# Optimization experiments

Hardware: AMD Instinct MI355X
Metric: run time of the kernel (lower is better)

The kernel has to match this reference:

```python
import jax, jax.numpy as jnp
import numpy as np
import math

B, N, W = 8, 2048, 512

def setup_inputs() -> dict:
    key0 = jax.random.key(0)
    ks = jax.random.split(key0, 6)
    return {
        "query": jax.random.normal(ks[0], (B, N, W), dtype=jnp.float32),
        "key":   jax.random.normal(ks[1], (B, N, W), dtype=jnp.float32),
        "W1": jax.random.normal(ks[2], (W, W), dtype=jnp.float32) * (1.0 / math.sqrt(W)),
        "b1": jax.random.normal(ks[3], (W,), dtype=jnp.float32) * 0.01,
        "W2": jax.random.normal(ks[4], (W, W), dtype=jnp.float32) * (1.0 / math.sqrt(W)),
        "b2": jax.random.normal(ks[5], (W,), dtype=jnp.float32) * 0.01,
    }

def _attn(q, k, v):
    # scores: [B, N, N]
    d_k = q.shape[-1]
    scores = jnp.einsum('bnd,bmd->bnm', q, k) / jnp.sqrt(jnp.asarray(d_k, q.dtype))
    p = jax.nn.softmax(scores, axis=-1)
    return jnp.einsum('bnm,bmd->bnd', p, v)

def reference(query, key, W1, b1, W2, b2):
    # nn.Linear: x @ W.T + b
    q = jnp.einsum('bnd,ed->bne', query, W1) + b1
    k = jnp.einsum('bnd,ed->bne', key, W2) + b2
    x1 = _attn(q, k, q)  # attention(query, key, query)
    x2 = _attn(k, q, k)  # attention(key, query, key)
    return jnp.concatenate((x1, x2), axis=1)  # [B, 2N, W]
```

## Files before the change

kernel.cpp:

```cpp
#include <hip/hip_runtime.h>
#include <hip/hip_bf16.h>
#include <stdint.h>

typedef unsigned short ushort_t;
typedef __attribute__((ext_vector_type(8))) short short8;
typedef __attribute__((ext_vector_type(4))) short short4v;
typedef __attribute__((ext_vector_type(4))) float f32x4;

__device__ inline ushort_t f2bf(float x) {
  uint32_t u = __float_as_uint(x);
  u += 0x7fffu + ((u >> 16) & 1u);
  return (ushort_t)(u >> 16);
}
__device__ inline float bfu2f(uint32_t h) { return __uint_as_float(h << 16); }

__device__ inline uint32_t pk2bf(float a, float b) {
  __hip_bfloat162 h = __float22bfloat162_rn(make_float2(a, b));
  union { __hip_bfloat162 h2; uint32_t u; } cv; cv.h2 = h; return cv.u;
}

__device__ inline void gload_lds16(const void* g, void* l) {
  __builtin_amdgcn_global_load_lds((const __attribute__((address_space(1))) uint32_t*)g,
                                   (__attribute__((address_space(3))) uint32_t*)l, 16, 0, 0);
}

__global__ __launch_bounds__(256) void linear_kernel(
    const float* __restrict__ query, const float* __restrict__ key,
    const float* __restrict__ W1, const float* __restrict__ b1,
    const float* __restrict__ W2, const float* __restrict__ b2,
    ushort_t* __restrict__ q_bf, ushort_t* __restrict__ k_bf,
    ushort_t* __restrict__ qT, ushort_t* __restrict__ kT)
{
  extern __shared__ __attribute__((aligned(16))) char smraw[];
  float*    smF = (float*)smraw;
  ushort_t* smU = (ushort_t*)smraw;

  int bx0 = blockIdx.x;
  int bx = ((bx0 & 7) << 7) | (bx0 >> 3);

  int which = bx >> 9, r2 = bx & 511, ct = r2 & 3, rt = r2 >> 2;
  const float* X    = which ? key : query;
  const float* Wm   = which ? W2  : W1;
  const float* bias = which ? b2  : b1;
  ushort_t* OUT  = which ? k_bf : q_bf;
  ushort_t* OUTT = which ? kT   : qT;

  int t = threadIdx.x, w = t >> 6, lane = t & 63, g = lane >> 4, m = lane & 15;
  int wr = (w >> 1) * 64, wc = (w & 1) * 64;
  int sr = lane >> 3, sp = lane & 7, sc = sp ^ sr;

  f32x4 zero = {0.f, 0.f, 0.f, 0.f};
  f32x4 acc[4][4];
#pragma unroll
  for (int i = 0; i < 4; ++i)
#pragma unroll
    for (int j = 0; j < 4; ++j) acc[i][j] = zero;

  auto stage = [&](int buf, int d0) {
    float* dst = smF + buf * 8192;
#pragma unroll
    for (int i = 0; i < 8; ++i) {
      int qi = w * 8 + i;
      const float* gsrc;
      float* ldst;
      if (qi < 16) {
        gsrc = X + (size_t)(rt * 128 + qi * 8 + sr) * 512 + d0 + sc * 4;
        ldst = dst + qi * 256;
      } else {
        int s = qi - 16;
        gsrc = Wm + (size_t)(ct * 128 + s * 8 + sr) * 512 + d0 + sc * 4;
        ldst = dst + 4096 + s * 256;
      }
      gload_lds16(gsrc, ldst);
    }
  };

  stage(0, 0);

  for (int it = 0; it < 16; ++it) {
    int cur = it & 1;
    __syncthreads();
    if (it + 1 < 16) stage(1 - cur, (it + 1) * 32);
    const float* bufF = smF + cur * 8192;

    short8 a4[4], b4[4];
#pragma unroll
    for (int i = 0; i < 4; ++i) {
      int row = wr + 16 * i + m, r8 = row & 7;
      int base = (row >> 3) * 256 + r8 * 32;
      f32x4 lo = *(const f32x4*)&bufF[base + (((2 * g)     ^ r8) * 4)];
      f32x4 hi = *(const f32x4*)&bufF[base + (((2 * g + 1) ^ r8) * 4)];
      union { uint32_t u[4]; short8 s; } fr;
      fr.u[0] = pk2bf(lo[0], lo[1]); fr.u[1] = pk2bf(lo[2], lo[3]);
      fr.u[2] = pk2bf(hi[0], hi[1]); fr.u[3] = pk2bf(hi[2], hi[3]);
      a4[i] = fr.s;
    }
#pragma unroll
    for (int j = 0; j < 4; ++j) {
      int row = wc + 16 * j + m, r8 = row & 7;
      int base = 4096 + (row >> 3) * 256 + r8 * 32;
      f32x4 lo = *(const f32x4*)&bufF[base + (((2 * g)     ^ r8) * 4)];
      f32x4 hi = *(const f32x4*)&bufF[base + (((2 * g + 1) ^ r8) * 4)];
      union { uint32_t u[4]; short8 s; } fr;
      fr.u[0] = pk2bf(lo[0], lo[1]); fr.u[1] = pk2bf(lo[2], lo[3]);
      fr.u[2] = pk2bf(hi[0], hi[1]); fr.u[3] = pk2bf(hi[2], hi[3]);
      b4[j] = fr.s;
    }
#pragma unroll
    for (int i = 0; i < 4; ++i)
#pragma unroll
      for (int j = 0; j < 4; ++j)
        acc[i][j] = __builtin_amdgcn_mfma_f32_16x16x32_bf16(a4[i], b4[j], acc[i][j], 0, 0, 0);
  }
  __syncthreads();

  float bw[4];
#pragma unroll
  for (int j = 0; j < 4; ++j) bw[j] = bias[ct * 128 + wc + 16 * j + m];

#pragma unroll
  for (int j = 0; j < 4; ++j)
#pragma unroll
    for (int i = 0; i < 4; ++i) {
      f32x4 c4 = acc[i][j];
#pragma unroll
      for (int rr = 0; rr < 4; ++rr)
        smU[(wr + 16 * i + 4 * g + rr) * 136 + wc + 16 * j + m] = f2bf(c4[rr] + bw[j]);
    }
  __syncthreads();
  {
    int row = t >> 1, half = t & 1;
    size_t gb = (size_t)(rt * 128 + row) * 512 + ct * 128 + half * 64;
#pragma unroll
    for (int i = 0; i < 8; ++i)
      *(short8*)(OUT + gb + i * 8) = *(const short8*)&smU[row * 136 + half * 64 + i * 8];
  }
  __syncthreads();

#pragma unroll
  for (int j = 0; j < 4; ++j)
#pragma unroll
    for (int i = 0; i < 4; ++i) {
      f32x4 c4 = acc[i][j];
      short4v tv;
#pragma unroll
      for (int rr = 0; rr < 4; ++rr) tv[rr] = (short)f2bf(c4[rr] + bw[j]);
      *(short4v*)&smU[(wc + 16 * j + m) * 136 + wr + 16 * i + 4 * g] = tv;
    }
  __syncthreads();
  {
    int cC = t >> 1, half = t & 1;
    size_t b_ = (size_t)(rt >> 4);
    size_t gb = b_ * (512 * 2048) + (size_t)(ct * 128 + cC) * 2048
              + (size_t)(rt & 15) * 128 + half * 64;
#pragma unroll
    for (int i = 0; i < 8; ++i)
      *(short8*)(OUTT + gb + i * 8) = *(const short8*)&smU[cC * 136 + half * 64 + i * 8];
  }
}

__global__ __launch_bounds__(512, 2) void attn_kernel(
    const ushort_t* __restrict__ qb, const ushort_t* __restrict__ kb_,
    const ushort_t* __restrict__ qT, const ushort_t* __restrict__ kT,
    float* __restrict__ out)
{
  extern __shared__ ushort_t sm[];
  const float CEXP = 1.4426950408889634f / 22.62741699796952f;

  int bx = blockIdx.x;
  int group = bx & 15, mtile = bx >> 4;
  int b = group >> 1, att = group & 1;
  const ushort_t* Qp = (att ? kb_ : qb) + (size_t)b * (2048 * 512);
  const ushort_t* Kp = (att ? qb  : kb_) + (size_t)b * (2048 * 512);
  const ushort_t* Vt = (att ? kT  : qT)  + (size_t)b * (512 * 2048);

  int t = threadIdx.x, w = t >> 6, lane = t & 63, g = lane >> 4, m = lane & 15;
  int wq = w >> 1, dh = w & 1;
  int qrow = mtile * 128 + w * 16 + m;
  int sw8  = ((g ^ ((m >> 1) & 3)) * 8);
  int srow = lane >> 2;
  int soff = ((lane & 3) ^ ((lane >> 3) & 3)) * 8;
  int pm6 = (m & 6);

  ushort_t* Plds = sm + 65536;
  float* lbuf = (float*)(sm + 69632);

  int pw0 = (w * 16 + m) * 32 + ((g ^ pm6) << 2);
  int pw1 = (w * 16 + m) * 32 + (((g + 4) ^ pm6) << 2);
  int pr0 = (wq * 32 +      m) * 32 + (((2 * g) ^ pm6) << 2);
  int pr1 = (wq * 32 + 16 + m) * 32 + (((2 * g) ^ pm6) << 2);

  short8 qf[16];
#pragma unroll
  for (int ks = 0; ks < 16; ++ks)
    qf[ks] = *(const short8*)(Qp + (size_t)qrow * 512 + ks * 32 + g * 8);

  f32x4 zero = {0.f, 0.f, 0.f, 0.f};
  f32x4 acc[16][2];
#pragma unroll
  for (int dt = 0; dt < 16; ++dt) { acc[dt][0] = zero; acc[dt][1] = zero; }
  float l = 0.f;

  auto stage = [&](int buf, int kb) {
    ushort_t* base = sm + buf * 32768;
    const int kbase = kb * 32;
#pragma unroll
    for (int i = 0; i < 4; ++i) {
      int qi = w * 4 + i, ks = qi >> 1, tt2 = qi & 1;
      const ushort_t* gsrc = Kp + (size_t)(kbase + tt2 * 16 + srow) * 512 + ks * 32 + soff;
      gload_lds16(gsrc, base + ks * 1024 + tt2 * 512);
    }
#pragma unroll
    for (int i = 0; i < 4; ++i) {
      int qi = w * 4 + i;
      const ushort_t* gsrc = Vt + (size_t)(qi * 16 + srow) * 2048 + kbase + soff;
      gload_lds16(gsrc, base + 16384 + qi * 512);
    }
  };

  stage(0, 0);

  for (int kb = 0; kb < 64; ++kb) {
    int cur = kb & 1;
    __syncthreads();
    if (kb + 1 < 64) stage(1 - cur, kb + 1);
    const ushort_t* base = sm + cur * 32768;

    f32x4 T0 = zero, T1 = zero;
    __builtin_amdgcn_s_setprio(1);
#pragma unroll
    for (int ks = 0; ks < 16; ++ks) {
      short8 k0 = *(const short8*)&base[ks * 1024 +       m * 32 + sw8];
      short8 k1 = *(const short8*)&base[ks * 1024 + 512 + m * 32 + sw8];
      T0 = __builtin_amdgcn_mfma_f32_16x16x32_bf16(k0, qf[ks], T0, 0, 0, 0);
      T1 = __builtin_amdgcn_mfma_f32_16x16x32_bf16(k1, qf[ks], T1, 0, 0, 0);
    }
    __builtin_amdgcn_s_setprio(0);

    uint32_t h[8];
#pragma unroll
    for (int r = 0; r < 4; ++r) {
      float e0 = __builtin_amdgcn_exp2f(T0[r] * CEXP);
      float e1 = __builtin_amdgcn_exp2f(T1[r] * CEXP);
      h[r]     = f2bf(e0);
      h[4 + r] = f2bf(e1);
      l += bfu2f(h[r]) + bfu2f(h[4 + r]);
    }
    uint2 p0, p1;
    p0.x = h[0] | (h[1] << 16); p0.y = h[2] | (h[3] << 16);
    p1.x = h[4] | (h[5] << 16); p1.y = h[6] | (h[7] << 16);
    *(uint2*)&Plds[pw0] = p0;
    *(uint2*)&Plds[pw1] = p1;

    __syncthreads();

    short8 pf0 = *(const short8*)&Plds[pr0];
    short8 pf1 = *(const short8*)&Plds[pr1];
    __builtin_amdgcn_s_setprio(1);
#pragma unroll
    for (int dt = 0; dt < 16; ++dt) {
      short8 vf = *(const short8*)&base[16384 + (dh * 16 + dt) * 512 + m * 32 + sw8];
      acc[dt][0] = __builtin_amdgcn_mfma_f32_16x16x32_bf16(vf, pf0, acc[dt][0], 0, 0, 0);
      acc[dt][1] = __builtin_amdgcn_mfma_f32_16x16x32_bf16(vf, pf1, acc[dt][1], 0, 0, 0);
    }
    __builtin_amdgcn_s_setprio(0);
  }

  l += __shfl_xor(l, 16, 64);
  l += __shfl_xor(l, 32, 64);
  if (lane < 16) lbuf[w * 16 + lane] = 1.0f / l;
  __syncthreads();

  float inv0 = lbuf[wq * 32 + m];
  float inv1 = lbuf[wq * 32 + 16 + m];
  size_t orow0 = (size_t)b * 4096 + (size_t)att * 2048 + mtile * 128 + wq * 32 + m;
  float* ob0 = out + orow0 * 512 + dh * 256;
  float* ob1 = out + (orow0 + 16) * 512 + dh * 256;
#pragma unroll
  for (int dt = 0; dt < 16; ++dt) {
    f32x4 v0 = acc[dt][0] * inv0;
    *(f32x4*)(ob0 + dt * 16 + g * 4) = v0;
  }
#pragma unroll
  for (int dt = 0; dt < 16; ++dt) {
    f32x4 v1 = acc[dt][1] * inv1;
    *(f32x4*)(ob1 + dt * 16 + g * 4) = v1;
  }
}

extern "C" void kernel_launch(void* const* d_in, const int* in_sizes, int n_in,
                              void* d_out, int out_size, void* d_ws, size_t ws_size,
                              hipStream_t stream) {
  const float* query = (const float*)d_in[0];
  const float* key   = (const float*)d_in[1];
  const float* W1    = (const float*)d_in[2];
  const float* b1    = (const float*)d_in[3];
  const float* W2    = (const float*)d_in[4];
  const float* b2    = (const float*)d_in[5];
  float* out = (float*)d_out;

  ushort_t* ws   = (ushort_t*)d_ws;
  ushort_t* q_bf = ws;
  ushort_t* k_bf = ws + 8388608;
  ushort_t* qT   = ws + 16777216;
  ushort_t* kT   = ws + 25165824;

  (void)hipFuncSetAttribute((const void*)linear_kernel,
                            hipFuncAttributeMaxDynamicSharedMemorySize, 65536);
  (void)hipFuncSetAttribute((const void*)attn_kernel,
                            hipFuncAttributeMaxDynamicSharedMemorySize, 139776);

  linear_kernel<<<1024, 256, 65536, stream>>>(query, key, W1, b1, W2, b2,
                                              q_bf, k_bf, qT, kT);
  attn_kernel<<<256, 512, 139776, stream>>>(q_bf, k_bf, qT, kT, out);
}
```

Before: 311.0 us.

## Software-pipeline PV of previous tile behind QK and retile PV per wave

Splits K and V staging into separate double buffers and double-buffers the P tile in LDS. Each iteration computes QK for the current key tile, then runs the P·V product of the previous tile, which removes the mid-iteration barrier between writing P and consuming it. The P·V work per wave changes from 16 d-tiles by 2 q-tiles to 8 d-tiles by 4 q-tiles, so each V fragment loaded from LDS feeds more MFMAs. The cost is more LDS, more accumulator and P-fragment registers, and an extra drain step after the loop.

```diff
diff --git a/kernel.cpp b/kernel.cpp
--- a/kernel.cpp
+++ b/kernel.cpp
@@ -175,20 +175,23 @@
   const ushort_t* Vt = (att ? kT  : qT)  + (size_t)b * (512 * 2048);
 
   int t = threadIdx.x, w = t >> 6, lane = t & 63, g = lane >> 4, m = lane & 15;
-  int wq = w >> 1, dh = w & 1;
+  int dq = w >> 1, qh = w & 1;
   int qrow = mtile * 128 + w * 16 + m;
   int sw8  = ((g ^ ((m >> 1) & 3)) * 8);
   int srow = lane >> 2;
   int soff = ((lane & 3) ^ ((lane >> 3) & 3)) * 8;
   int pm6 = (m & 6);
 
-  ushort_t* Plds = sm + 65536;
-  float* lbuf = (float*)(sm + 69632);
+  ushort_t* Plds = sm + 131072 / 2 * 2;
+  float* lbuf = (float*)(sm + 73728);
+  (void)Plds;
 
   int pw0 = (w * 16 + m) * 32 + ((g ^ pm6) << 2);
   int pw1 = (w * 16 + m) * 32 + (((g + 4) ^ pm6) << 2);
-  int pr0 = (wq * 32 +      m) * 32 + (((2 * g) ^ pm6) << 2);
-  int pr1 = (wq * 32 + 16 + m) * 32 + (((2 * g) ^ pm6) << 2);
+  int prq[4];
+#pragma unroll
+  for (int qt = 0; qt < 4; ++qt)
+    prq[qt] = (qh * 64 + qt * 16 + m) * 32 + (((2 * g) ^ pm6) << 2);
 
   short8 qf[16];
 #pragma unroll
@@ -196,46 +199,73 @@
     qf[ks] = *(const short8*)(Qp + (size_t)qrow * 512 + ks * 32 + g * 8);
 
   f32x4 zero = {0.f, 0.f, 0.f, 0.f};
-  f32x4 acc[16][2];
-#pragma unroll
-  for (int dt = 0; dt < 16; ++dt) { acc[dt][0] = zero; acc[dt][1] = zero; }
+  f32x4 acc[8][4];
+#pragma unroll
+  for (int dt = 0; dt < 8; ++dt)
+#pragma unroll
+    for (int qt = 0; qt < 4; ++qt) acc[dt][qt] = zero;
   float l = 0.f;
 
-  auto stage = [&](int buf, int kb) {
-    ushort_t* base = sm + buf * 32768;
-    const int kbase = kb * 32;
+  auto stageK = [&](int buf, int kt) {
+    ushort_t* base = sm + buf * 16384;
+    const int kbase = kt * 32;
 #pragma unroll
     for (int i = 0; i < 4; ++i) {
       int qi = w * 4 + i, ks = qi >> 1, tt2 = qi & 1;
       const ushort_t* gsrc = Kp + (size_t)(kbase + tt2 * 16 + srow) * 512 + ks * 32 + soff;
       gload_lds16(gsrc, base + ks * 1024 + tt2 * 512);
     }
+  };
+  auto stageV = [&](int buf, int kt) {
+    ushort_t* base = sm + 32768 + buf * 16384;
+    const int kbase = kt * 32;
 #pragma unroll
     for (int i = 0; i < 4; ++i) {
       int qi = w * 4 + i;
       const ushort_t* gsrc = Vt + (size_t)(qi * 16 + srow) * 2048 + kbase + soff;
-      gload_lds16(gsrc, base + 16384 + qi * 512);
+      gload_lds16(gsrc, base + qi * 512);
     }
   };
 
-  stage(0, 0);
+  auto pv = [&](int pt) {
+    int pb = pt & 1;
+    const ushort_t* vb = sm + 32768 + pb * 16384;
+    const ushort_t* pp = sm + 65536 + pb * 4096;
+    short8 pf[4];
+#pragma unroll
+    for (int qt = 0; qt < 4; ++qt) pf[qt] = *(const short8*)&pp[prq[qt]];
+    __builtin_amdgcn_s_setprio(1);
+#pragma unroll
+    for (int dt = 0; dt < 8; ++dt) {
+      short8 vf = *(const short8*)&vb[(dq * 8 + dt) * 512 + m * 32 + sw8];
+#pragma unroll
+      for (int qt = 0; qt < 4; ++qt)
+        acc[dt][qt] = __builtin_amdgcn_mfma_f32_16x16x32_bf16(vf, pf[qt], acc[dt][qt], 0, 0, 0);
+    }
+    __builtin_amdgcn_s_setprio(0);
+  };
+
+  stageK(0, 0);
 
   for (int kb = 0; kb < 64; ++kb) {
     int cur = kb & 1;
     __syncthreads();
-    if (kb + 1 < 64) stage(1 - cur, kb + 1);
-    const ushort_t* base = sm + cur * 32768;
-
+    if (kb + 1 < 64) stageK(1 - cur, kb + 1);
+    stageV(cur, kb);
+
+    const ushort_t* kbuf = sm + cur * 16384;
     f32x4 T0 = zero, T1 = zero;
     __builtin_amdgcn_s_setprio(1);
 #pragma unroll
     for (int ks = 0; ks < 16; ++ks) {
-      short8 k0 = *(const short8*)&base[ks * 1024 +       m * 32 + sw8];
-      short8 k1 = *(const short8*)&base[ks * 1024 + 512 + m * 32 + sw8];
+      short8 k0 = *(const short8*)&kbuf[ks * 1024 +       m * 32 + sw8];
+      short8 k1 = *(const short8*)&kbuf[ks * 1024 + 512 + m * 32 + sw8];
       T0 = __builtin_amdgcn_mfma_f32_16x16x32_bf16(k0, qf[ks], T0, 0, 0, 0);
       T1 = __builtin_amdgcn_mfma_f32_16x16x32_bf16(k1, qf[ks], T1, 0, 0, 0);
     }
     __builtin_amdgcn_s_setprio(0);
+
+    if (kb > 0) pv(kb - 1);
 
     uint32_t h[8];
 #pragma unroll
@@ -249,42 +279,30 @@
     uint2 p0, p1;
     p0.x = h[0] | (h[1] << 16); p0.y = h[2] | (h[3] << 16);
     p1.x = h[4] | (h[5] << 16); p1.y = h[6] | (h[7] << 16);
-    *(uint2*)&Plds[pw0] = p0;
-    *(uint2*)&Plds[pw1] = p1;
-
-    __syncthreads();
-
-    short8 pf0 = *(const short8*)&Plds[pr0];
-    short8 pf1 = *(const short8*)&Plds[pr1];
-    __builtin_amdgcn_s_setprio(1);
-#pragma unroll
-    for (int dt = 0; dt < 16; ++dt) {
-      short8 vf = *(const short8*)&base[16384 + (dh * 16 + dt) * 512 + m * 32 + sw8];
-      acc[dt][0] = __builtin_amdgcn_mfma_f32_16x16x32_bf16(vf, pf0, acc[dt][0], 0, 0, 0);
-      acc[dt][1] = __builtin_amdgcn_mfma_f32_16x16x32_bf16(vf, pf1, acc[dt][1], 0, 0, 0);
-    }
-    __builtin_amdgcn_s_setprio(0);
+    ushort_t* pwb = sm + 65536 + cur * 4096;
+    *(uint2*)&pwb[pw0] = p0;
+    *(uint2*)&pwb[pw1] = p1;
   }
 
   l += __shfl_xor(l, 16, 64);
   l += __shfl_xor(l, 32, 64);
   if (lane < 16) lbuf[w * 16 + lane] = 1.0f / l;
-  __syncthreads();
-
-  float inv0 = lbuf[wq * 32 + m];
-  float inv1 = lbuf[wq * 32 + 16 + m];
-  size_t orow0 = (size_t)b * 4096 + (size_t)att * 2048 + mtile * 128 + wq * 32 + m;
-  float* ob0 = out + orow0 * 512 + dh * 256;
-  float* ob1 = out + (orow0 + 16) * 512 + dh * 256;
-#pragma unroll
-  for (int dt = 0; dt < 16; ++dt) {
-    f32x4 v0 = acc[dt][0] * inv0;
-    *(f32x4*)(ob0 + dt * 16 + g * 4) = v0;
-  }
-#pragma unroll
-  for (int dt = 0; dt < 16; ++dt) {
-    f32x4 v1 = acc[dt][1] * inv1;
-    *(f32x4*)(ob1 + dt * 16 + g * 4) = v1;
+
+  __syncthreads();
+  pv(63);
+
+  float inv[4];
+#pragma unroll
+  for (int qt = 0; qt < 4; ++qt) inv[qt] = lbuf[qh * 64 + qt * 16 + m];
+  size_t orow = (size_t)b * 4096 + (size_t)att * 2048 + mtile * 128 + qh * 64 + m;
+#pragma unroll
+  for (int qt = 0; qt < 4; ++qt) {
+    float* ob = out + (orow + qt * 16) * 512 + dq * 128;
+#pragma unroll
+    for (int dt = 0; dt < 8; ++dt) {
+      f32x4 v = acc[dt][qt] * inv[qt];
+      *(f32x4*)(ob + dt * 16 + g * 4) = v;
+    }
   }
 }
 
@@ -308,9 +326,9 @@
   (void)hipFuncSetAttribute((const void*)linear_kernel,
                             hipFuncAttributeMaxDynamicSharedMemorySize, 65536);
   (void)hipFuncSetAttribute((const void*)attn_kernel,
-                            hipFuncAttributeMaxDynamicSharedMemorySize, 139776);
+                            hipFuncAttributeMaxDynamicSharedMemorySize, 147968);
 
   linear_kernel<<<1024, 256, 65536, stream>>>(query, key, W1, b1, W2, b2,
                                               q_bf, k_bf, qT, kT);
-  attn_kernel<<<256, 512, 139776, stream>>>(q_bf, k_bf, qT, kT, out);
-}
+  attn_kernel<<<256, 512, 147968, stream>>>(q_bf, k_bf, qT, kT, out);
+}
```

Result: slower. 327.6 us (+5.3%).

## Restructure linear kernel to full-width 128x512 tiles with X staged once in LDS

Applied to the files above, without the earlier changes.

The projection kernel now gives each block 128 rows times all 512 output columns with 512 threads. The X tile is converted to bf16 once and held in swizzled LDS, while each wave reads its W rows straight from global memory every k-step. This removes the fourfold re-reading and re-conversion of X across column tiles and the double-buffered staging pipeline. In exchange the grid shrinks to 256 blocks, LDS use grows to about 136 KB, W loads are no longer prefetched, and register pressure rises with 32 accumulators per wave.

```diff
diff --git a/kernel.cpp b/kernel.cpp
--- a/kernel.cpp
+++ b/kernel.cpp
@@ -24,21 +24,17 @@
                                    (__attribute__((address_space(3))) uint32_t*)l, 16, 0, 0);
 }
 
-__global__ __launch_bounds__(256) void linear_kernel(
+__global__ __launch_bounds__(512, 2) void linear_kernel(
     const float* __restrict__ query, const float* __restrict__ key,
     const float* __restrict__ W1, const float* __restrict__ b1,
     const float* __restrict__ W2, const float* __restrict__ b2,
     ushort_t* __restrict__ q_bf, ushort_t* __restrict__ k_bf,
     ushort_t* __restrict__ qT, ushort_t* __restrict__ kT)
 {
-  extern __shared__ __attribute__((aligned(16))) char smraw[];
-  float*    smF = (float*)smraw;
-  ushort_t* smU = (ushort_t*)smraw;
-
-  int bx0 = blockIdx.x;
-  int bx = ((bx0 & 7) << 7) | (bx0 >> 3);
-
-  int which = bx >> 9, r2 = bx & 511, ct = r2 & 3, rt = r2 >> 2;
+  extern __shared__ __attribute__((aligned(16))) ushort_t smL[];
+
+  int bx = blockIdx.x;
+  int which = bx & 1, rt = bx >> 1;
   const float* X    = which ? key : query;
   const float* Wm   = which ? W2  : W1;
   const float* bias = which ? b2  : b1;
@@ -46,116 +42,100 @@
   ushort_t* OUTT = which ? kT   : qT;
 
   int t = threadIdx.x, w = t >> 6, lane = t & 63, g = lane >> 4, m = lane & 15;
-  int wr = (w >> 1) * 64, wc = (w & 1) * 64;
-  int sr = lane >> 3, sp = lane & 7, sc = sp ^ sr;
+
+  {
+    int tp = t & 127, rsub = t >> 7;
+#pragma unroll 4
+    for (int p = 0; p < 32; ++p) {
+      int row = p * 4 + rsub;
+      f32x4 v = *(const f32x4*)(X + (size_t)(rt * 128 + row) * 512 + tp * 4);
+      uint2 dv;
+      dv.x = pk2bf(v[0], v[1]);
+      dv.y = pk2bf(v[2], v[3]);
+      int chunk = tp >> 1;
+      int phys = chunk ^ (row & 7);
+      *(uint2*)&smL[row * 512 + phys * 8 + (tp & 1) * 4] = dv;
+    }
+  }
+  __syncthreads();
 
   f32x4 zero = {0.f, 0.f, 0.f, 0.f};
-  f32x4 acc[4][4];
-#pragma unroll
-  for (int i = 0; i < 4; ++i)
+  f32x4 acc[8][4];
+#pragma unroll
+  for (int i = 0; i < 8; ++i)
 #pragma unroll
     for (int j = 0; j < 4; ++j) acc[i][j] = zero;
 
-  auto stage = [&](int buf, int d0) {
-    float* dst = smF + buf * 8192;
+  const float* Wbase = Wm + (size_t)(w * 64) * 512;
+
+  for (int k0 = 0; k0 < 16; ++k0) {
+    short8 bfr[4];
+#pragma unroll
+    for (int j = 0; j < 4; ++j) {
+      const float* wp = Wbase + (size_t)(16 * j + m) * 512 + k0 * 32 + g * 8;
+      f32x4 lo = *(const f32x4*)wp;
+      f32x4 hi = *(const f32x4*)(wp + 4);
+      union { uint32_t u[4]; short8 s; } fb;
+      fb.u[0] = pk2bf(lo[0], lo[1]); fb.u[1] = pk2bf(lo[2], lo[3]);
+      fb.u[2] = pk2bf(hi[0], hi[1]); fb.u[3] = pk2bf(hi[2], hi[3]);
+      bfr[j] = fb.s;
+    }
+    short8 afr[8];
 #pragma unroll
     for (int i = 0; i < 8; ++i) {
-      int qi = w * 8 + i;
-      const float* gsrc;
-      float* ldst;
-      if (qi < 16) {
-        gsrc = X + (size_t)(rt * 128 + qi * 8 + sr) * 512 + d0 + sc * 4;
-        ldst = dst + qi * 256;
-      } else {
-        int s = qi - 16;
-        gsrc = Wm + (size_t)(ct * 128 + s * 8 + sr) * 512 + d0 + sc * 4;
-        ldst = dst + 4096 + s * 256;
-      }
-      gload_lds16(gsrc, ldst);
-    }
-  };
-
-  stage(0, 0);
-
-  for (int it = 0; it < 16; ++it) {
-    int cur = it & 1;
-    __syncthreads();
-    if (it + 1 < 16) stage(1 - cur, (it + 1) * 32);
-    const float* bufF = smF + cur * 8192;
-
-    short8 a4[4], b4[4];
-#pragma unroll
-    for (int i = 0; i < 4; ++i) {
-      int row = wr + 16 * i + m, r8 = row & 7;
-      int base = (row >> 3) * 256 + r8 * 32;
-      f32x4 lo = *(const f32x4*)&bufF[base + (((2 * g)     ^ r8) * 4)];
-      f32x4 hi = *(const f32x4*)&bufF[base + (((2 * g + 1) ^ r8) * 4)];
-      union { uint32_t u[4]; short8 s; } fr;
-      fr.u[0] = pk2bf(lo[0], lo[1]); fr.u[1] = pk2bf(lo[2], lo[3]);
-      fr.u[2] = pk2bf(hi[0], hi[1]); fr.u[3] = pk2bf(hi[2], hi[3]);
-      a4[i] = fr.s;
-    }
-#pragma unroll
-    for (int j = 0; j < 4; ++j) {
-      int row = wc + 16 * j + m, r8 = row & 7;
-      int base = 4096 + (row >> 3) * 256 + r8 * 32;
-      f32x4 lo = *(const f32x4*)&bufF[base + (((2 * g)     ^ r8) * 4)];
-      f32x4 hi = *(const f32x4*)&bufF[base + (((2 * g + 1) ^ r8) * 4)];
-      union { uint32_t u[4]; short8 s; } fr;
-      fr.u[0] = pk2bf(lo[0], lo[1]); fr.u[1] = pk2bf(lo[2], lo[3]);
-      fr.u[2] = pk2bf(hi[0], hi[1]); fr.u[3] = pk2bf(hi[2], hi[3]);
-      b4[j] = fr.s;
-    }
-#pragma unroll
-    for (int i = 0; i < 4; ++i)
+      int row = 16 * i + m;
+      int phys = (k0 * 4 + g) ^ (m & 7);
+      afr[i] = *(const short8*)&smL[row * 512 + phys * 8];
+    }
+#pragma unroll
+    for (int i = 0; i < 8; ++i)
 #pragma unroll
       for (int j = 0; j < 4; ++j)
-        acc[i][j] = __builtin_amdgcn_mfma_f32_16x16x32_bf16(a4[i], b4[j], acc[i][j], 0, 0, 0);
-  }
-  __syncthreads();
+        acc[i][j] = __builtin_amdgcn_mfma_f32_16x16x32_bf16(afr[i], bfr[j], acc[i][j], 0, 0, 0);
+  }
 
   float bw[4];
 #pragma unroll
-  for (int j = 0; j < 4; ++j) bw[j] = bias[ct * 128 + wc + 16 * j + m];
+  for (int j = 0; j < 4; ++j) bw[j] = bias[w * 64 + 16 * j + m];
+
+  __syncthreads();
 
 #pragma unroll
   for (int j = 0; j < 4; ++j)
 #pragma unroll
-    for (int i = 0; i < 4; ++i) {
+    for (int i = 0; i < 8; ++i) {
       f32x4 c4 = acc[i][j];
 #pragma unroll
       for (int rr = 0; rr < 4; ++rr)
-        smU[(wr + 16 * i + 4 * g + rr) * 136 + wc + 16 * j + m] = f2bf(c4[rr] + bw[j]);
+        smL[(16 * i + 4 * g + rr) * 520 + w * 64 + 16 * j + m] = f2bf(c4[rr] + bw[j]);
     }
   __syncthreads();
   {
-    int row = t >> 1, half = t & 1;
-    size_t gb = (size_t)(rt * 128 + row) * 512 + ct * 128 + half * 64;
-#pragma unroll
-    for (int i = 0; i < 8; ++i)
-      *(short8*)(OUT + gb + i * 8) = *(const short8*)&smU[row * 136 + half * 64 + i * 8];
+    int row = t >> 2, qtr = t & 3;
+    size_t gb = (size_t)(rt * 128 + row) * 512 + qtr * 128;
+#pragma unroll
+    for (int i2 = 0; i2 < 16; ++i2)
+      *(short8*)(OUT + gb + i2 * 8) = *(const short8*)&smL[row * 520 + qtr * 128 + i2 * 8];
   }
   __syncthreads();
 
 #pragma unroll
   for (int j = 0; j < 4; ++j)
 #pragma unroll
-    for (int i = 0; i < 4; ++i) {
+    for (int i = 0; i < 8; ++i) {
       f32x4 c4 = acc[i][j];
       short4v tv;
 #pragma unroll
       for (int rr = 0; rr < 4; ++rr) tv[rr] = (short)f2bf(c4[rr] + bw[j]);
-      *(short4v*)&smU[(wc + 16 * j + m) * 136 + wr + 16 * i + 4 * g] = tv;
+      *(short4v*)&smL[(w * 64 + 16 * j + m) * 136 + 16 * i + 4 * g] = tv;
     }
   __syncthreads();
   {
-    int cC = t >> 1, half = t & 1;
     size_t b_ = (size_t)(rt >> 4);
-    size_t gb = b_ * (512 * 2048) + (size_t)(ct * 128 + cC) * 2048
-              + (size_t)(rt & 15) * 128 + half * 64;
-#pragma unroll
-    for (int i = 0; i < 8; ++i)
-      *(short8*)(OUTT + gb + i * 8) = *(const short8*)&smU[cC * 136 + half * 64 + i * 8];
+    size_t gb = b_ * (512 * 2048) + (size_t)t * 2048 + (size_t)(rt & 15) * 128;
+#pragma unroll
+    for (int i2 = 0; i2 < 16; ++i2)
+      *(short8*)(OUTT + gb + i2 * 8) = *(const short8*)&smL[t * 136 + i2 * 8];
   }
 }
 
@@ -306,11 +286,11 @@
   ushort_t* kT   = ws + 25165824;
 
   (void)hipFuncSetAttribute((const void*)linear_kernel,
-                            hipFuncAttributeMaxDynamicSharedMemorySize, 65536);
+                            hipFuncAttributeMaxDynamicSharedMemorySize, 139264);
   (void)hipFuncSetAttribute((const void*)attn_kernel,
                             hipFuncAttributeMaxDynamicSharedMemorySize, 139776);
 
-  linear_kernel<<<1024, 256, 65536, stream>>>(query, key, W1, b1, W2, b2,
+  linear_kernel<<<256, 512, 139264, stream>>>(query, key, W1, b1, W2, b2,
                                               q_bf, k_bf, qT, kT);
   attn_kernel<<<256, 512, 139776, stream>>>(q_bf, k_bf, qT, kT, out);
 }
```

After: 320.9 us. +3.2%, slower.
